# Kernel optimization log

Hardware: AMD Instinct MI355X
Metric: run time of the kernel (lower is better)

Reference implementation:

```python
import jax, jax.numpy as jnp
import numpy as np

T, B, I, H, O = 2048, 128, 32, 128, 1


def setup_inputs() -> dict:
    key = jax.random.key(0)
    ks = jax.random.split(key, 5)
    X = jax.random.normal(ks[0], (T, B, I), dtype=jnp.float32)
    W_in = jax.random.normal(ks[1], (H, I), dtype=jnp.float32) / np.sqrt(I)
    W_hh = jax.random.normal(ks[2], (H, H), dtype=jnp.float32) / np.sqrt(H)
    rnn_bias = jnp.zeros((H,), dtype=jnp.float32)
    alpha = jax.random.uniform(ks[3], (H,), dtype=jnp.float32)
    value_W = jax.random.normal(ks[4], (O, H), dtype=jnp.float32) / np.sqrt(H)
    value_bias = jnp.zeros((O,), dtype=jnp.float32)
    return {"X": X, "W_in": W_in, "W_hh": W_hh, "rnn_bias": rnn_bias,
            "alpha": alpha, "value_W": value_W, "value_bias": value_bias}


def reference(X, W_in, W_hh, rnn_bias, alpha, value_W, value_bias):
    # X: (T, B, I). Precompute input projections for all timesteps at once.
    xproj = jnp.einsum('tbi,hi->tbh', X, W_in)  # (T, B, H)

    def step(h_prev, xp_t):
        h_tilde = jnp.tanh(xp_t + h_prev @ W_hh.T + rnn_bias)
        h = (1.0 - alpha) * h_prev + alpha * h_tilde  # per-unit leaky blend
        return h, h

    h0 = jnp.zeros((X.shape[1], W_hh.shape[0]), dtype=X.dtype)
    last_hidden, Z = jax.lax.scan(step, h0, xproj)  # Z: (T, B, H)
    V = value_bias + jnp.einsum('tbh,oh->tbo', Z, value_W)  # (T, B, O)
    return V, last_hidden
```

## Files before the change

### kernel.cpp

```cpp
#include <hip/hip_runtime.h>
#include <hip/hip_fp16.h>

#define TT 2048
#define BB 128
#define II 32
#define HH 128
#define NW (TT / 8)

typedef float v2f __attribute__((ext_vector_type(2)));
typedef float v4f __attribute__((ext_vector_type(4)));
typedef unsigned int u32;

__device__ __forceinline__ v2f pk_fma(v2f a, v2f b, v2f c) {
    v2f d;
    asm("v_pk_fma_f32 %0, %1, %2, %3" : "=v"(d) : "v"(a), "v"(b), "v"(c));
    return d;
}
template <int CTRL>
__device__ __forceinline__ float dpp_mov(float p) {
    return __int_as_float(__builtin_amdgcn_update_dpp(0, __float_as_int(p), CTRL, 0xF, 0xF, true));
}
template <int CTRL>
__device__ __forceinline__ float dpp_add(float p) { return p + dpp_mov<CTRL>(p); }
template <int CTRL>
__device__ __forceinline__ float pair_red(float x, float y, bool sel) {
    float keep = sel ? y : x;
    float give = sel ? x : y;
    return keep + dpp_mov<CTRL>(give);
}
__device__ __forceinline__ void unpack2(u32 u, float& lo, float& hi) {
    lo = __half2float(__ushort_as_half((unsigned short)u));
    hi = __half2float(__ushort_as_half((unsigned short)(u >> 16)));
}

__global__ __launch_bounds__(256, 1)
void vrnn_kernel(const float* __restrict__ X, const float* __restrict__ W_in,
                 const float* __restrict__ W_hh, const float* __restrict__ rnn_bias,
                 const float* __restrict__ alpha, const float* __restrict__ value_W,
                 const float* __restrict__ value_bias, float* __restrict__ out)
{
    const int b    = blockIdx.x;
    const int tid  = threadIdx.x;
    const int wave = tid >> 6;
    const int lane = tid & 63;
    const int g    = lane >> 4;
    const int j    = lane & 15;
    const int base = 32 * wave + 8 * g;
    const int rown = base + (j & 7);

    __shared__ __align__(16) __half hbuf[2][160];
    __shared__ __align__(16) float  vres[TT];

    v2f xa[8], xb[8];
#pragma unroll
    for (int s = 0; s < 8; ++s)
        xa[s] = *(const v2f*)(X + (size_t)s * (BB * II) + b * II + 2 * j);

    const float SC = 2.8853900817779268f;

    v2f wh[8][4], wi8[8], binit[8];
#pragma unroll
    for (int r = 0; r < 8; ++r) {
        const float* wr = W_hh + (size_t)(base + r) * HH + 8 * j;
        v4f a0 = *(const v4f*)(wr);
        v4f a1 = *(const v4f*)(wr + 4);
        wh[r][0] = (v2f){a0.x * SC, a0.y * SC}; wh[r][1] = (v2f){a0.z * SC, a0.w * SC};
        wh[r][2] = (v2f){a1.x * SC, a1.y * SC}; wh[r][3] = (v2f){a1.z * SC, a1.w * SC};
        v2f wiv  = *(const v2f*)(W_in + (size_t)(base + r) * II + 2 * j);
        wi8[r]   = (v2f){wiv.x * SC, wiv.y * SC};
        binit[r] = (v2f){ (j == 0) ? rnn_bias[base + r] * SC : 0.0f, 0.0f };
    }
    v2f vwc[4];
#pragma unroll
    for (int i = 0; i < 4; ++i) vwc[i] = *(const v2f*)(value_W + 8 * j + 2 * i);
    const float al_own = alpha[rown];
    const float vb     = value_bias[0];
    const bool  b0 = (j & 1) != 0;
    const bool  b1 = (j & 2) != 0;
    const bool  b2 = (j & 4) != 0;
    const int   roff_h = 8 * j + 16 * (j >> 3);
    const int   woff_h = 8 * (rown >> 3) + 16 * (rown >> 6) + (rown & 7);

    float hreg = 0.0f;
    float hpre = 0.0f;

    if (tid < 160) ((u32*)hbuf)[tid] = 0u;
    __syncthreads();

    float* outV = out;
    float* outH = out + (size_t)TT * BB;

#define STEP(W_, S_, XARR)                                                     \
    {                                                                          \
        const int t   = 8 * (W_) + (S_);                                       \
        const int par = (S_) & 1;                                              \
        const __half* hb = &hbuf[par ^ 1][roff_h];                             \
        const v4f hv = *(const v4f*)hb;                                        \
        float h0, h1, h2, h3, h4, h5, h6, h7;                                  \
        unpack2(__float_as_uint(hv.x), h0, h1);                                \
        unpack2(__float_as_uint(hv.y), h2, h3);                                \
        unpack2(__float_as_uint(hv.z), h4, h5);                                \
        unpack2(__float_as_uint(hv.w), h6, h7);                                \
        v2f hp[4] = { (v2f){h0, h1}, (v2f){h2, h3},                            \
                      (v2f){h4, h5}, (v2f){h6, h7} };                          \
        float p[8];                                                            \
        _Pragma("unroll")                                                      \
        for (int r = 0; r < 8; ++r) {                                          \
            v2f a = pk_fma(wi8[r], XARR[S_], binit[r]);                        \
            a = pk_fma(wh[r][0], hp[0], a);                                    \
            a = pk_fma(wh[r][1], hp[1], a);                                    \
            a = pk_fma(wh[r][2], hp[2], a);                                    \
            a = pk_fma(wh[r][3], hp[3], a);                                    \
            p[r] = a.x + a.y;                                                  \
        }                                                                      \
        float q0 = pair_red<0xB1>(p[0], p[1], b0);                             \
        float q1 = pair_red<0xB1>(p[2], p[3], b0);                             \
        float q2 = pair_red<0xB1>(p[4], p[5], b0);                             \
        float q3 = pair_red<0xB1>(p[6], p[7], b0);                             \
        float r0 = pair_red<0x4E>(q0, q1, b1);                                 \
        float r1 = pair_red<0x4E>(q2, q3, b1);                                 \
        const float k3 = b2 ? r1 : r0;                                         \
        const float g3 = b2 ? r0 : r1;                                         \
        const float vL = dpp_mov<0x104>(g3);                                   \
        const float vR = dpp_mov<0x114>(g3);                                   \
        float pre = k3 + (b2 ? vR : vL);                                       \
        pre += dpp_mov<0x128>(pre);                                            \
        const float e  = __builtin_amdgcn_exp2f(pre);                          \
        const float rc = __builtin_amdgcn_rcpf(e + 1.0f);                      \
        const float gt = fmaf(-2.0f, rc, 1.0f);                                \
        hreg = fmaf(al_own, gt, hpre);                                         \
        hbuf[par][woff_h] = __float2half(hreg);                                \
        hpre = fmaf(-al_own, hreg, hreg);                                      \
        if (wave == ((S_) & 3) && t > 0) {                                     \
            v2f vt = vwc[0] * hp[0];                                           \
            vt = pk_fma(vwc[1], hp[1], vt);                                    \
            vt = pk_fma(vwc[2], hp[2], vt);                                    \
            vt = pk_fma(vwc[3], hp[3], vt);                                    \
            float vs = vt.x + vt.y;                                            \
            vs = dpp_add<0xB1>(vs);                                            \
            vs = dpp_add<0x4E>(vs);                                            \
            const float uL = dpp_mov<0x104>(vs);                               \
            const float uR = dpp_mov<0x114>(vs);                               \
            vs += b2 ? uR : uL;                                                \
            vs = dpp_add<0x128>(vs);                                           \
            if (lane == 0) vres[t - 1] = vb + vs;                              \
        }                                                                      \
        asm volatile("s_waitcnt lgkmcnt(0)" ::: "memory");                     \
        __builtin_amdgcn_s_barrier();                                          \
    }

    for (int w2 = 0; w2 < NW; w2 += 2) {
#pragma unroll
        for (int s = 0; s < 8; ++s) {
            const int trow = 8 * (w2 + 1) + s;
            xb[s] = *(const v2f*)(X + (size_t)trow * (BB * II) + b * II + 2 * j);
        }
#pragma unroll
        for (int s = 0; s < 8; ++s) STEP(w2, s, xa)
#pragma unroll
        for (int s = 0; s < 8; ++s) {
            int trow = 8 * (w2 + 2) + s;
            if (trow > TT - 1) trow = TT - 1;
            xa[s] = *(const v2f*)(X + (size_t)trow * (BB * II) + b * II + 2 * j);
        }
#pragma unroll
        for (int s = 0; s < 8; ++s) STEP(w2 + 1, s, xb)
    }
#undef STEP

    if (wave == 0) {
        const __half* hb = &hbuf[1][roff_h];
        const v4f hv = *(const v4f*)hb;
        float h0, h1, h2, h3, h4, h5, h6, h7;
        unpack2(__float_as_uint(hv.x), h0, h1);
        unpack2(__float_as_uint(hv.y), h2, h3);
        unpack2(__float_as_uint(hv.z), h4, h5);
        unpack2(__float_as_uint(hv.w), h6, h7);
        v2f hp[4] = { (v2f){h0, h1}, (v2f){h2, h3},
                      (v2f){h4, h5}, (v2f){h6, h7} };
        v2f vt = vwc[0] * hp[0];
        vt = pk_fma(vwc[1], hp[1], vt);
        vt = pk_fma(vwc[2], hp[2], vt);
        vt = pk_fma(vwc[3], hp[3], vt);
        float vs = vt.x + vt.y;
        vs = dpp_add<0xB1>(vs);
        vs = dpp_add<0x4E>(vs);
        const float uL = dpp_mov<0x104>(vs);
        const float uR = dpp_mov<0x114>(vs);
        vs += b2 ? uR : uL;
        vs = dpp_add<0x128>(vs);
        if (lane == 0) vres[TT - 1] = vb + vs;
    }
    if (j < 8)
        outH[(size_t)b * HH + rown] = hreg;
    __syncthreads();
#pragma unroll
    for (int i = 0; i < TT / 256; ++i)
        outV[(size_t)(i * 256 + tid) * BB + b] = vres[i * 256 + tid];
}

extern "C" void kernel_launch(void* const* d_in, const int* in_sizes, int n_in,
                              void* d_out, int out_size, void* d_ws, size_t ws_size,
                              hipStream_t stream) {
    const float* X      = (const float*)d_in[0];
    const float* W_in   = (const float*)d_in[1];
    const float* W_hh   = (const float*)d_in[2];
    const float* rbias  = (const float*)d_in[3];
    const float* alpha  = (const float*)d_in[4];
    const float* vW     = (const float*)d_in[5];
    const float* vbias  = (const float*)d_in[6];
    float* out = (float*)d_out;

    vrnn_kernel<<<dim3(BB), dim3(256), 0, stream>>>(X, W_in, W_hh, rbias, alpha, vW, vbias, out);
}
```

Measured before the change: 830.7 us.

## Stage X via async global-to-LDS loads, keep h in fp32, precompute input term

Wave 0 now streams each block of 8 timesteps of X directly into a double-buffered LDS tile with global_load_lds, so the per-lane register arrays holding X go away. The input projection for the next step is computed after the current step's barrier work, taking it off the recurrence's critical path. The hidden state is now stored in LDS as fp32 with a padded layout, removing the fp16 pack/unpack. The row-shift reduction uses row_shr DPP adds plus a select instead of a cross-row swap, and the leaky tanh update is folded into a single FMA. In exchange it adds a vmcnt wait on wave 0 each window and relies on the new LDS layout and lane-to-row mapping being consistent.

```diff
diff --git a/kernel.cpp b/kernel.cpp
--- a/kernel.cpp
+++ b/kernel.cpp
@@ -1,5 +1,4 @@
 #include <hip/hip_runtime.h>
-#include <hip/hip_fp16.h>
 
 #define TT 2048
 #define BB 128
@@ -10,6 +9,8 @@
 typedef float v2f __attribute__((ext_vector_type(2)));
 typedef float v4f __attribute__((ext_vector_type(4)));
 typedef unsigned int u32;
+typedef __attribute__((address_space(3))) u32 lds_u32;
+typedef const __attribute__((address_space(1))) u32 glb_u32;
 
 __device__ __forceinline__ v2f pk_fma(v2f a, v2f b, v2f c) {
     v2f d;
@@ -28,12 +29,8 @@
     float give = sel ? x : y;
     return keep + dpp_mov<CTRL>(give);
 }
-__device__ __forceinline__ void unpack2(u32 u, float& lo, float& hi) {
-    lo = __half2float(__ushort_as_half((unsigned short)u));
-    hi = __half2float(__ushort_as_half((unsigned short)(u >> 16)));
-}
-
-__global__ __launch_bounds__(256, 1)
+
+__global__ __launch_bounds__(256)
 void vrnn_kernel(const float* __restrict__ X, const float* __restrict__ W_in,
                  const float* __restrict__ W_hh, const float* __restrict__ rnn_bias,
                  const float* __restrict__ alpha, const float* __restrict__ value_W,
@@ -46,15 +43,15 @@
     const int g    = lane >> 4;
     const int j    = lane & 15;
     const int base = 32 * wave + 8 * g;
-    const int rown = base + (j & 7);
-
-    __shared__ __align__(16) __half hbuf[2][160];
-    __shared__ __align__(16) float  vres[TT];
-
-    v2f xa[8], xb[8];
-#pragma unroll
-    for (int s = 0; s < 8; ++s)
-        xa[s] = *(const v2f*)(X + (size_t)s * (BB * II) + b * II + 2 * j);
+
+    __shared__ __align__(16) float xw[2][8][II];
+    __shared__ __align__(16) float hbuf[2][192];
+    __shared__ __align__(16) float vres[TT];
+
+    if (wave == 0) {
+        const float* src = X + (size_t)(lane >> 3) * (BB * II) + b * II + (lane & 7) * 4;
+        __builtin_amdgcn_global_load_lds((glb_u32*)src, (lds_u32*)(&xw[0][0][0]), 16, 0, 0);
+    }
 
     const float SC = 2.8853900817779268f;
 
@@ -73,40 +70,50 @@
     v2f vwc[4];
 #pragma unroll
     for (int i = 0; i < 4; ++i) vwc[i] = *(const v2f*)(value_W + 8 * j + 2 * i);
-    const float al_own = alpha[rown];
-    const float vb     = value_bias[0];
     const bool  b0 = (j & 1) != 0;
     const bool  b1 = (j & 2) != 0;
-    const bool  b2 = (j & 4) != 0;
-    const int   roff_h = 8 * j + 16 * (j >> 3);
-    const int   woff_h = 8 * (rown >> 3) + 16 * (rown >> 6) + (rown & 7);
+    const bool  selhi = ((j >> 2) & 1) != 0;
+    const int   rown2 = base + (j & 3) + 4 * ((j >> 2) & 1);
+    const float al_own = alpha[rown2];
+    const float nal2   = -2.0f * al_own;
+    const float oneml  = 1.0f - al_own;
+    const float vb     = value_bias[0];
+    const int   woff = 12 * (4 * wave + g) + (j & 3) + 4 * ((j >> 2) & 1);
 
     float hreg = 0.0f;
-    float hpre = 0.0f;
-
-    if (tid < 160) ((u32*)hbuf)[tid] = 0u;
+    float hsum = al_own;
+    v2f   xc_next;
+    v2f   pinit[8];
+
+    if (tid < 192) hbuf[1][tid] = 0.0f;
     __syncthreads();
 
     float* outV = out;
     float* outH = out + (size_t)TT * BB;
 
-#define STEP(W_, S_, XARR)                                                     \
+#define STEP(S_)                                                               \
     {                                                                          \
-        const int t   = 8 * (W_) + (S_);                                       \
+        const int t   = 8 * w + (S_);                                          \
         const int par = (S_) & 1;                                              \
-        const __half* hb = &hbuf[par ^ 1][roff_h];                             \
-        const v4f hv = *(const v4f*)hb;                                        \
-        float h0, h1, h2, h3, h4, h5, h6, h7;                                  \
-        unpack2(__float_as_uint(hv.x), h0, h1);                                \
-        unpack2(__float_as_uint(hv.y), h2, h3);                                \
-        unpack2(__float_as_uint(hv.z), h4, h5);                                \
-        unpack2(__float_as_uint(hv.w), h6, h7);                                \
-        v2f hp[4] = { (v2f){h0, h1}, (v2f){h2, h3},                            \
-                      (v2f){h4, h5}, (v2f){h6, h7} };                          \
+                                    \
+        const float* hb = &hbuf[par ^ 1][12 * j];                              \
+        const v4f h0v = *(const v4f*)(hb);                                     \
+        const v4f h1v = *(const v4f*)(hb + 4);                                 \
+        v2f pin[8];                                                            \
+        if ((S_) == 0) {                                                       \
+            const v2f xc0 = *(const v2f*)(&xw[w & 1][0][2 * j]);               \
+            _Pragma("unroll")                                                  \
+            for (int r = 0; r < 8; ++r) pin[r] = pk_fma(wi8[r], xc0, binit[r]);\
+        } else {                                                               \
+            _Pragma("unroll")                                                  \
+            for (int r = 0; r < 8; ++r) pin[r] = pinit[r];                     \
+        }                                                                      \
+        v2f hp[4] = { (v2f){h0v.x, h0v.y}, (v2f){h0v.z, h0v.w},                \
+                      (v2f){h1v.x, h1v.y}, (v2f){h1v.z, h1v.w} };              \
         float p[8];                                                            \
         _Pragma("unroll")                                                      \
         for (int r = 0; r < 8; ++r) {                                          \
-            v2f a = pk_fma(wi8[r], XARR[S_], binit[r]);                        \
+            v2f a = pin[r];                                                    \
             a = pk_fma(wh[r][0], hp[0], a);                                    \
             a = pk_fma(wh[r][1], hp[1], a);                                    \
             a = pk_fma(wh[r][2], hp[2], a);                                    \
@@ -119,19 +126,16 @@
         float q3 = pair_red<0xB1>(p[6], p[7], b0);                             \
         float r0 = pair_red<0x4E>(q0, q1, b1);                                 \
         float r1 = pair_red<0x4E>(q2, q3, b1);                                 \
-        const float k3 = b2 ? r1 : r0;                                         \
-        const float g3 = b2 ? r0 : r1;                                         \
-        const float vL = dpp_mov<0x104>(g3);                                   \
-        const float vR = dpp_mov<0x114>(g3);                                   \
-        float pre = k3 + (b2 ? vR : vL);                                       \
-        pre += dpp_mov<0x128>(pre);                                            \
+        r0 = dpp_add<0x124>(r0);  r1 = dpp_add<0x124>(r1);                     \
+        r0 = dpp_add<0x128>(r0);  r1 = dpp_add<0x128>(r1);                     \
+        const float pre = selhi ? r1 : r0;                                     \
         const float e  = __builtin_amdgcn_exp2f(pre);                          \
         const float rc = __builtin_amdgcn_rcpf(e + 1.0f);                      \
-        const float gt = fmaf(-2.0f, rc, 1.0f);                                \
-        hreg = fmaf(al_own, gt, hpre);                                         \
-        hbuf[par][woff_h] = __float2half(hreg);                                \
-        hpre = fmaf(-al_own, hreg, hreg);                                      \
-        if (wave == ((S_) & 3) && t > 0) {                                     \
+        hreg = fmaf(nal2, rc, hsum);                                           \
+        hbuf[par][woff] = hreg;                                                \
+                                                          \
+        hsum = fmaf(oneml, hreg, al_own);                                      \
+        if (wave == ((S_) & 3) && ((w | (S_)) != 0)) {                         \
             v2f vt = vwc[0] * hp[0];                                           \
             vt = pk_fma(vwc[1], hp[1], vt);                                    \
             vt = pk_fma(vwc[2], hp[2], vt);                                    \
@@ -139,45 +143,39 @@
             float vs = vt.x + vt.y;                                            \
             vs = dpp_add<0xB1>(vs);                                            \
             vs = dpp_add<0x4E>(vs);                                            \
-            const float uL = dpp_mov<0x104>(vs);                               \
-            const float uR = dpp_mov<0x114>(vs);                               \
-            vs += b2 ? uR : uL;                                                \
+            vs = dpp_add<0x124>(vs);                                           \
             vs = dpp_add<0x128>(vs);                                           \
             if (lane == 0) vres[t - 1] = vb + vs;                              \
         }                                                                      \
+        if ((S_) < 7) {                                                        \
+            xc_next = *(const v2f*)(&xw[w & 1][(S_) + 1][2 * j]);              \
+            _Pragma("unroll")                                                  \
+            for (int r = 0; r < 8; ++r)                                        \
+                pinit[r] = pk_fma(wi8[r], xc_next, binit[r]);                  \
+        }                                                                      \
+        if (wave == 0 && (S_) == 7)                                            \
+            asm volatile("s_waitcnt vmcnt(0)" ::: "memory");                   \
         asm volatile("s_waitcnt lgkmcnt(0)" ::: "memory");                     \
         __builtin_amdgcn_s_barrier();                                          \
     }
 
-    for (int w2 = 0; w2 < NW; w2 += 2) {
-#pragma unroll
-        for (int s = 0; s < 8; ++s) {
-            const int trow = 8 * (w2 + 1) + s;
-            xb[s] = *(const v2f*)(X + (size_t)trow * (BB * II) + b * II + 2 * j);
+    for (int w = 0; w < NW; ++w) {
+        if (wave == 0 && w + 1 < NW) {
+            const float* src = X + (size_t)((w + 1) * 8 + (lane >> 3)) * (BB * II)
+                                 + b * II + (lane & 7) * 4;
+            __builtin_amdgcn_global_load_lds((glb_u32*)src,
+                (lds_u32*)(&xw[(w + 1) & 1][0][0]), 16, 0, 0);
         }
-#pragma unroll
-        for (int s = 0; s < 8; ++s) STEP(w2, s, xa)
-#pragma unroll
-        for (int s = 0; s < 8; ++s) {
-            int trow = 8 * (w2 + 2) + s;
-            if (trow > TT - 1) trow = TT - 1;
-            xa[s] = *(const v2f*)(X + (size_t)trow * (BB * II) + b * II + 2 * j);
-        }
-#pragma unroll
-        for (int s = 0; s < 8; ++s) STEP(w2 + 1, s, xb)
+        STEP(0) STEP(1) STEP(2) STEP(3) STEP(4) STEP(5) STEP(6) STEP(7)
     }
 #undef STEP
 
     if (wave == 0) {
-        const __half* hb = &hbuf[1][roff_h];
-        const v4f hv = *(const v4f*)hb;
-        float h0, h1, h2, h3, h4, h5, h6, h7;
-        unpack2(__float_as_uint(hv.x), h0, h1);
-        unpack2(__float_as_uint(hv.y), h2, h3);
-        unpack2(__float_as_uint(hv.z), h4, h5);
-        unpack2(__float_as_uint(hv.w), h6, h7);
-        v2f hp[4] = { (v2f){h0, h1}, (v2f){h2, h3},
-                      (v2f){h4, h5}, (v2f){h6, h7} };
+        const float* hb = &hbuf[1][12 * j];
+        const v4f h0v = *(const v4f*)(hb);
+        const v4f h1v = *(const v4f*)(hb + 4);
+        v2f hp[4] = { (v2f){h0v.x, h0v.y}, (v2f){h0v.z, h0v.w},
+                      (v2f){h1v.x, h1v.y}, (v2f){h1v.z, h1v.w} };
         v2f vt = vwc[0] * hp[0];
         vt = pk_fma(vwc[1], hp[1], vt);
         vt = pk_fma(vwc[2], hp[2], vt);
@@ -185,14 +183,12 @@
         float vs = vt.x + vt.y;
         vs = dpp_add<0xB1>(vs);
         vs = dpp_add<0x4E>(vs);
-        const float uL = dpp_mov<0x104>(vs);
-        const float uR = dpp_mov<0x114>(vs);
-        vs += b2 ? uR : uL;
+        vs = dpp_add<0x124>(vs);
         vs = dpp_add<0x128>(vs);
         if (lane == 0) vres[TT - 1] = vb + vs;
     }
     if (j < 8)
-        outH[(size_t)b * HH + rown] = hreg;
+        outH[(size_t)b * HH + base + j] = hreg;
     __syncthreads();
 #pragma unroll
     for (int i = 0; i < TT / 256; ++i)
```

Result: faster. 770.2 us (-7.3%).
